# Kernel optimization log

Hardware: AMD Instinct MI355X
Metric: run time of the kernel (lower is better)

## Reference

```python
import jax, jax.numpy as jnp
import numpy as np

D = 1024      # d_model
ED = 2048     # d_inner
K = 4         # d_conv
N = 16        # d_state
R = 64        # dt_rank
E = 8         # num_experts
TOPK = 2      # num_experts_per_tok
FF = 2048     # mlp_size
EPS = 1e-6
B, L = 1, 2048


def setup_inputs() -> dict:
    key = jax.random.key(0)
    ks = jax.random.split(key, 12)
    def nrm(k, shape, scale=0.02):
        return jax.random.normal(k, shape, jnp.float32) * scale
    return {
        "x": jax.random.normal(ks[0], (B, L, D), jnp.float32),
        "rms1_w": jnp.ones((D,), jnp.float32),
        "rms2_w": jnp.ones((D,), jnp.float32),
        "W_in": nrm(ks[1], (2 * ED, D)),
        "conv_w": nrm(ks[2], (ED, 1, K), 0.1),
        "conv_b": jnp.zeros((ED,), jnp.float32),
        "W_xproj": nrm(ks[3], (R + 2 * N, ED)),
        "W_dt": nrm(ks[4], (ED, R), 0.1),
        "b_dt": jnp.full((ED,), -4.6, jnp.float32),  # softplus(-4.6) ~ 0.01 init dt
        "A_log": jnp.log(jnp.tile(jnp.arange(1, N + 1, dtype=jnp.float32), (ED, 1))),  # S4D-real init
        "D_skip": jnp.ones((ED,), jnp.float32),
        "W_out": nrm(ks[5], (D, ED)),
        "W_router": nrm(ks[6], (E, D)),
        "gate_w": nrm(ks[7], (E, FF, D)),
        "up_w": nrm(ks[8], (E, FF, D)),
        "down_w": nrm(ks[9], (E, D, FF)),
    }


def rmsnorm(x, w):
    return x * jax.lax.rsqrt(jnp.mean(x * x, -1, keepdims=True) + EPS) * w


def mamba(x, W_in, conv_w, conv_b, W_xproj, W_dt, b_dt, A_log, D_skip, W_out):
    Bb, Ll, _ = x.shape
    xm, z = jnp.split(x @ W_in.T, 2, axis=-1)                 # [B,L,ED] each
    # depthwise causal conv over time
    xc = jax.lax.conv_general_dilated(xm.transpose(0, 2, 1), conv_w, (1,), [(K - 1, 0)],
                                      feature_group_count=ED)  # [B,ED,L]
    xc = jax.nn.silu((xc + conv_b[None, :, None]).transpose(0, 2, 1))  # [B,L,ED]
    dt, Bm, Cm = jnp.split(xc @ W_xproj.T, [R, R + N], axis=-1)        # [B,L,R],[B,L,N],[B,L,N]
    delta = jax.nn.softplus(dt @ W_dt.T + b_dt)                        # [B,L,ED]
    A = -jnp.exp(A_log)                                                # [ED,N]
    dA = jnp.exp(delta[..., None] * A)                                 # [B,L,ED,N]
    dBx = delta[..., None] * Bm[:, :, None, :] * xc[..., None]         # [B,L,ED,N]

    def step(h, t):
        dA_t, dBx_t, C_t = t
        h = dA_t * h + dBx_t
        return h, jnp.einsum("ben,bn->be", h, C_t)

    h0 = jnp.zeros((Bb, ED, N), x.dtype)
    _, ys = jax.lax.scan(step, h0, (dA.transpose(1, 0, 2, 3), dBx.transpose(1, 0, 2, 3), Cm.transpose(1, 0, 2)))
    y = ys.transpose(1, 0, 2) + D_skip * xc
    y = y * jax.nn.silu(z)
    return y @ W_out.T


def moe(x2d, W_router, gate_w, up_w, down_w):
    logits = x2d @ W_router.T                                  # [T,E]
    probs = jax.nn.softmax(logits.astype(jnp.float32), -1)
    topw, sel = jax.lax.top_k(probs, TOPK)                     # NOTE: no renormalization (faithful)
    topw = topw.astype(x2d.dtype)
    wmat = jnp.sum(jax.nn.one_hot(sel, E, dtype=x2d.dtype) * topw[..., None], axis=1)  # [T,E]
    g = jnp.einsum("td,efd->tef", x2d, gate_w)
    u = jnp.einsum("td,efd->tef", x2d, up_w)
    h = jax.nn.silu(g) * u
    ye = jnp.einsum("tef,edf->ted", h, down_w)
    out = jnp.einsum("ted,te->td", ye, wmat)
    return out, logits


def reference(x, rms1_w, rms2_w, W_in, conv_w, conv_b, W_xproj, W_dt, b_dt, A_log,
              D_skip, W_out, W_router, gate_w, up_w, down_w):
    Bb, Ll, Dd = x.shape
    res = x
    h = rmsnorm(x, rms1_w)
    h = mamba(h, W_in, conv_w, conv_b, W_xproj, W_dt, b_dt, A_log, D_skip, W_out)
    x = res + h
    res = x
    h = rmsnorm(x, rms2_w)
    mo, logits = moe(h.reshape(-1, Dd), W_router, gate_w, up_w, down_w)
    x = res + mo.reshape(Bb, Ll, Dd)
    return (x, logits)
```

## Files before the change

### kernel.cpp

```cpp
#include <hip/hip_runtime.h>
#include <math.h>

typedef unsigned short u16;
typedef unsigned int   u32;
typedef __attribute__((ext_vector_type(8))) short bf16x8;
typedef __attribute__((ext_vector_type(4))) float f32x4;

constexpr int Tn=2048, Dm=1024, EDc=2048, Ns=16, Rr=64, NEx=8, FFc=2048;
constexpr int SCH=32, SNCH=Tn/SCH;
constexpr int MAXTM=40;
constexpr float LOG2E = 1.44269504f;

__device__ __forceinline__ float siluf(float x){ return __fdividef(x, 1.f + __expf(-x)); }
__device__ __forceinline__ u16 bfr(float f){
  u32 u = __float_as_uint(f);
  return (u16)((u + 0x7fffu + ((u>>16)&1u)) >> 16);
}
__device__ __forceinline__ float b2f(u16 h){ return __uint_as_float(((u32)h)<<16); }

__device__ __forceinline__ void gload16(const void* g, void* l){
  __builtin_amdgcn_global_load_lds((const __attribute__((address_space(1))) void*)g,
                                   (__attribute__((address_space(3))) void*)l, 16, 0, 0);
}

__global__ __launch_bounds__(256) void f2b_k(const float* __restrict__ in,
                                             u16* __restrict__ out, int n4){
  int i = blockIdx.x*256 + threadIdx.x;
  if (i >= n4) return;
  float4 v = ((const float4*)in)[i];
  u32 lo = (u32)bfr(v.x) | ((u32)bfr(v.y)<<16);
  u32 hi = (u32)bfr(v.z) | ((u32)bfr(v.w)<<16);
  ((uint2*)out)[i] = make_uint2(lo, hi);
}

__global__ __launch_bounds__(256) void f2b3_k(
    const float* __restrict__ g, const float* __restrict__ u,
    const float* __restrict__ d,
    u16* __restrict__ og, u16* __restrict__ ou, u16* __restrict__ od){
  const int BPW = (NEx*FFc*Dm/4)/256;
  int b = blockIdx.x;
  int which = b / BPW;
  int i = (b - which*BPW)*256 + threadIdx.x;
  const float* in = (which==0) ? g : (which==1) ? u : d;
  u16* out        = (which==0) ? og : (which==1) ? ou : od;
  float4 v = ((const float4*)in)[i];
  u32 lo = (u32)bfr(v.x) | ((u32)bfr(v.y)<<16);
  u32 hi = (u32)bfr(v.z) | ((u32)bfr(v.w)<<16);
  ((uint2*)out)[i] = make_uint2(lo, hi);
}

__global__ __launch_bounds__(256) void rmsnorm_k(const float* __restrict__ x,
                                                 const float* __restrict__ w,
                                                 u16* __restrict__ ob){
  int t = blockIdx.x;
  const float* xr = x + (size_t)t * Dm;
  float v[4]; float s = 0.f;
#pragma unroll
  for (int j = 0; j < 4; j++){ int d = threadIdx.x + j*256; v[j] = xr[d]; s += v[j]*v[j]; }
#pragma unroll
  for (int m = 1; m < 64; m <<= 1) s += __shfl_xor(s, m);
  __shared__ float red[4]; __shared__ float sb;
  int lane = threadIdx.x & 63, wv = threadIdx.x >> 6;
  if (lane == 0) red[wv] = s;
  __syncthreads();
  if (threadIdx.x == 0) sb = rsqrtf((red[0]+red[1]+red[2]+red[3]) * (1.f/Dm) + 1e-6f);
  __syncthreads();
  float sc = sb;
#pragma unroll
  for (int j = 0; j < 4; j++){
    int d = threadIdx.x + j*256;
    ob[(size_t)t*Dm + d] = bfr(v[j]*sc*w[d]);
  }
}

__global__ __launch_bounds__(256) void rms2red_k(
  const float* __restrict__ x, const float* __restrict__ P,
  const float* __restrict__ w,
  float* __restrict__ out, float* __restrict__ h2f, u16* __restrict__ h2b)
{
  int t = blockIdx.x, tid = threadIdx.x;
  const size_t S = (size_t)Tn*Dm;
  float v[4]; float s = 0.f;
#pragma unroll
  for (int j = 0; j < 4; j++){
    int d = tid + j*256;
    size_t idx = (size_t)t*Dm + d;
    float a = x[idx] + ((P[idx] + P[S+idx]) + (P[2*S+idx] + P[3*S+idx]));
    out[idx] = a; v[j] = a; s += a*a;
  }
#pragma unroll
  for (int m = 1; m < 64; m <<= 1) s += __shfl_xor(s, m);
  __shared__ float red[4]; __shared__ float sb;
  int lane = tid & 63, wv = tid >> 6;
  if (lane == 0) red[wv] = s;
  __syncthreads();
  if (tid == 0) sb = rsqrtf((red[0]+red[1]+red[2]+red[3]) * (1.f/Dm) + 1e-6f);
  __syncthreads();
  float sc = sb;
#pragma unroll
  for (int j = 0; j < 4; j++){
    int d = tid + j*256;
    float o = v[j]*sc*w[d];
    h2b[(size_t)t*Dm + d] = bfr(o);
    h2f[(size_t)t*Dm + d] = o;
  }
}

template<int EPI, int OB>
__global__ __launch_bounds__(512) void gemm_bb(
    const u16* __restrict__ A, int lda,
    const u16* __restrict__ B, int ldb,
    void* __restrict__ Cv, int ldc,
    int M, int N, int Ksl, const float* __restrict__ aux)
{
  __shared__ u16 As[2*4096], Bs[2*4096];
  int tid = threadIdx.x, lane = tid & 63, wid = tid >> 6;
  int wr = wid >> 2, wc = wid & 3;
  int n0 = blockIdx.x * 128, m0 = blockIdx.y * 128;
  int r = tid >> 2;
  int kk = ((tid & 3) ^ (r & 3)) * 8;
  size_t kbeg = (size_t)blockIdx.z * Ksl;
  const u16* Ag = A + (size_t)min(m0 + r, M-1)*lda + kbeg + kk;
  const u16* Bg = B + (size_t)min(n0 + r, N-1)*ldb + kbeg + kk;
  f32x4 acc[4][2] = {};
  int sw = ((lane>>4) ^ (lane&3)) * 8;
  int aoff[4], boff[2];
#pragma unroll
  for (int i = 0; i < 4; i++) aoff[i] = (wr*64 + i*16 + (lane&15))*32 + sw;
#pragma unroll
  for (int j = 0; j < 2; j++) boff[j] = (wc*32 + j*16 + (lane&15))*32 + sw;
  gload16(Ag, As + tid*8);
  gload16(Bg, Bs + tid*8);
  int NT = Ksl >> 5;
  for (int kt = 0; kt < NT; kt++){
    int cur = (kt & 1) * 4096;
    if (kt + 1 < NT){
      int nxt = 4096 - cur;
      gload16(Ag + (size_t)(kt+1)*32, As + nxt + tid*8);
      gload16(Bg + (size_t)(kt+1)*32, Bs + nxt + tid*8);
      asm volatile("s_waitcnt vmcnt(2)" ::: "memory");
    } else {
      asm volatile("s_waitcnt vmcnt(0)" ::: "memory");
    }
    __builtin_amdgcn_s_barrier();
    bf16x8 af[4], bv[2];
#pragma unroll
    for (int i = 0; i < 4; i++) af[i] = *(const bf16x8*)&As[cur + aoff[i]];
#pragma unroll
    for (int j = 0; j < 2; j++) bv[j] = *(const bf16x8*)&Bs[cur + boff[j]];
    asm volatile("s_waitcnt lgkmcnt(0)" ::: "memory");
    __builtin_amdgcn_sched_barrier(0);
    __builtin_amdgcn_s_barrier();
    __builtin_amdgcn_s_setprio(1);
#pragma unroll
    for (int i = 0; i < 4; i++)
#pragma unroll
      for (int j = 0; j < 2; j++)
        acc[i][j] = __builtin_amdgcn_mfma_f32_16x16x32_bf16(af[i], bv[j], acc[i][j], 0,0,0);
    __builtin_amdgcn_s_setprio(0);
  }
  float* Cf = (float*)Cv + (size_t)blockIdx.z * M * ldc;
  u16*   Cb = (u16*)Cv;
#pragma unroll
  for (int i = 0; i < 4; i++){
    int rbase = m0 + wr*64 + i*16 + ((lane>>4)<<2);
#pragma unroll
    for (int j = 0; j < 2; j++){
      int col = n0 + wc*32 + j*16 + (lane&15);
      if (col >= N) continue;
#pragma unroll
      for (int q = 0; q < 4; q++){
        int row = rbase + q;
        if (row >= M) continue;
        float v = acc[i][j][q];
        if (EPI == 1){ v += aux[col]; v = (v > 20.f) ? v : __logf(1.f + __expf(v)); }
        if (OB) Cb[(size_t)row*ldc + col] = bfr(v);
        else    Cf[(size_t)row*ldc + col] = v;
      }
    }
  }
}

__global__ __launch_bounds__(512) void gateup8(
    const u16* __restrict__ Aall,
    const u16* __restrict__ Wg, const u16* __restrict__ Wu,
    const int* __restrict__ cnt, const int* __restrict__ off,
    const int* __restrict__ bucket,
    const int* __restrict__ tmap, const int* __restrict__ ntot,
    u16* __restrict__ H)
{
  if ((int)blockIdx.y >= *ntot) return;
  int v = tmap[blockIdx.y];
  int e = v >> 16, m0 = (v & 0xFFFF) * 128;
  int Me = cnt[e];
  __shared__ u16 As[3*4096], Gs[3*4096], Us[3*4096];
  int tid = threadIdx.x, lane = tid & 63, wid = tid >> 6;
  int wr = wid >> 2, wc = wid & 3;
  int n0 = blockIdx.x * 128;
  int r = tid >> 2;
  int kk = ((tid & 3) ^ (r & 3)) * 8;
  int arow = bucket[e*Tn + min(m0 + r, Me-1)];
  const u16* Ag = Aall + (size_t)arow*Dm + kk;
  const u16* Gg = Wg + ((size_t)e*FFc + n0 + r)*Dm + kk;
  const u16* Ug = Wu + ((size_t)e*FFc + n0 + r)*Dm + kk;
  f32x4 ag[4][2] = {}, au[4][2] = {};
  int sw = ((lane>>4) ^ (lane&3)) * 8;
  int aoff[4], boff[2];
#pragma unroll
  for (int i = 0; i < 4; i++) aoff[i] = (wr*64 + i*16 + (lane&15))*32 + sw;
#pragma unroll
  for (int j = 0; j < 2; j++) boff[j] = (wc*32 + j*16 + (lane&15))*32 + sw;
  gload16(Ag,      As + tid*8);
  gload16(Gg,      Gs + tid*8);
  gload16(Ug,      Us + tid*8);
  gload16(Ag + 32, As + 4096 + tid*8);
  gload16(Gg + 32, Gs + 4096 + tid*8);
  gload16(Ug + 32, Us + 4096 + tid*8);
  const int NT = Dm >> 5;
  int cur = 0;
  for (int kt = 0; kt < NT; kt++){
    if (kt + 2 < NT){
      int nx2 = cur + 2*4096; if (nx2 >= 3*4096) nx2 -= 3*4096;
      gload16(Ag + (size_t)(kt+2)*32, As + nx2 + tid*8);
      gload16(Gg + (size_t)(kt+2)*32, Gs + nx2 + tid*8);
      gload16(Ug + (size_t)(kt+2)*32, Us + nx2 + tid*8);
      asm volatile("s_waitcnt vmcnt(6)" ::: "memory");
    } else if (kt + 1 < NT){
      asm volatile("s_waitcnt vmcnt(3)" ::: "memory");
    } else {
      asm volatile("s_waitcnt vmcnt(0)" ::: "memory");
    }
    __builtin_amdgcn_s_barrier();
    bf16x8 af[4], gf[2], uf[2];
#pragma unroll
    for (int i = 0; i < 4; i++) af[i] = *(const bf16x8*)&As[cur + aoff[i]];
#pragma unroll
    for (int j = 0; j < 2; j++){ gf[j] = *(const bf16x8*)&Gs[cur + boff[j]];
                                 uf[j] = *(const bf16x8*)&Us[cur + boff[j]]; }
    asm volatile("s_waitcnt lgkmcnt(0)" ::: "memory");
    __builtin_amdgcn_sched_barrier(0);
    __builtin_amdgcn_s_barrier();
    __builtin_amdgcn_s_setprio(1);
#pragma unroll
    for (int i = 0; i < 4; i++)
#pragma unroll
      for (int j = 0; j < 2; j++){
        ag[i][j] = __builtin_amdgcn_mfma_f32_16x16x32_bf16(af[i], gf[j], ag[i][j], 0,0,0);
        au[i][j] = __builtin_amdgcn_mfma_f32_16x16x32_bf16(af[i], uf[j], au[i][j], 0,0,0);
      }
    __builtin_amdgcn_s_setprio(0);
    cur += 4096; if (cur >= 3*4096) cur -= 3*4096;
  }
  int offe = off[e];
#pragma unroll
  for (int i = 0; i < 4; i++){
    int mb = m0 + wr*64 + i*16 + ((lane>>4)<<2);
#pragma unroll
    for (int j = 0; j < 2; j++){
      int col = n0 + wc*32 + j*16 + (lane&15);
#pragma unroll
      for (int q = 0; q < 4; q++){
        int m = mb + q;
        if (m >= Me) continue;
        float g = ag[i][j][q], u = au[i][j][q];
        H[(size_t)(offe + m)*FFc + col] = bfr(siluf(g)*u);
      }
    }
  }
}

__global__ __launch_bounds__(512) void down8(
    const u16* __restrict__ Hall, const u16* __restrict__ Wd,
    const int* __restrict__ cnt, const int* __restrict__ off,
    const int* __restrict__ tmap, const int* __restrict__ ntot,
    u16* __restrict__ Y)
{
  if ((int)blockIdx.y >= *ntot) return;
  int v = tmap[blockIdx.y];
  int e = v >> 16, m0 = (v & 0xFFFF) * 128;
  int Me = cnt[e];
  int offe = off[e];
  int kbeg = blockIdx.z * (FFc/2);
  const u16* A = Hall + (size_t)offe*FFc;
  const u16* B = Wd + (size_t)e*Dm*FFc;
  u16* C = Y + (size_t)blockIdx.z*(2*Tn)*Dm + (size_t)offe*Dm;
  __shared__ u16 As[3*4096], Bs[3*4096];
  int tid = threadIdx.x, lane = tid & 63, wid = tid >> 6;
  int wr = wid >> 2, wc = wid & 3;
  int n0 = blockIdx.x * 128;
  int r = tid >> 2;
  int kk = ((tid & 3) ^ (r & 3)) * 8;
  const u16* Ag = A + (size_t)min(m0 + r, Me-1)*FFc + kbeg + kk;
  const u16* Bg = B + (size_t)(n0 + r)*FFc + kbeg + kk;
  f32x4 acc[4][2] = {};
  int sw = ((lane>>4) ^ (lane&3)) * 8;
  int aoff[4], boff[2];
#pragma unroll
  for (int i = 0; i < 4; i++) aoff[i] = (wr*64 + i*16 + (lane&15))*32 + sw;
#pragma unroll
  for (int j = 0; j < 2; j++) boff[j] = (wc*32 + j*16 + (lane&15))*32 + sw;
  gload16(Ag,      As + tid*8);
  gload16(Bg,      Bs + tid*8);
  gload16(Ag + 32, As + 4096 + tid*8);
  gload16(Bg + 32, Bs + 4096 + tid*8);
  const int NT = (FFc/2) >> 5;
  int cur = 0;
  for (int kt = 0; kt < NT; kt++){
    if (kt + 2 < NT){
      int nx2 = cur + 2*4096; if (nx2 >= 3*4096) nx2 -= 3*4096;
      gload16(Ag + (size_t)(kt+2)*32, As + nx2 + tid*8);
      gload16(Bg + (size_t)(kt+2)*32, Bs + nx2 + tid*8);
      asm volatile("s_waitcnt vmcnt(4)" ::: "memory");
    } else if (kt + 1 < NT){
      asm volatile("s_waitcnt vmcnt(2)" ::: "memory");
    } else {
      asm volatile("s_waitcnt vmcnt(0)" ::: "memory");
    }
    __builtin_amdgcn_s_barrier();
    bf16x8 af[4], bv[2];
#pragma unroll
    for (int i = 0; i < 4; i++) af[i] = *(const bf16x8*)&As[cur + aoff[i]];
#pragma unroll
    for (int j = 0; j < 2; j++) bv[j] = *(const bf16x8*)&Bs[cur + boff[j]];
    asm volatile("s_waitcnt lgkmcnt(0)" ::: "memory");
    __builtin_amdgcn_sched_barrier(0);
    __builtin_amdgcn_s_barrier();
    __builtin_amdgcn_s_setprio(1);
#pragma unroll
    for (int i = 0; i < 4; i++)
#pragma unroll
      for (int j = 0; j < 2; j++)
        acc[i][j] = __builtin_amdgcn_mfma_f32_16x16x32_bf16(af[i], bv[j], acc[i][j], 0,0,0);
    __builtin_amdgcn_s_setprio(0);
    cur += 4096; if (cur >= 3*4096) cur -= 3*4096;
  }
#pragma unroll
  for (int i = 0; i < 4; i++){
    int mb = m0 + wr*64 + i*16 + ((lane>>4)<<2);
#pragma unroll
    for (int j = 0; j < 2; j++){
      int col = n0 + wc*32 + j*16 + (lane&15);
#pragma unroll
      for (int q = 0; q < 4; q++){
        int m = mb + q;
        if (m >= Me) continue;
        C[(size_t)m*Dm + col] = bfr(acc[i][j][q]);
      }
    }
  }
}

__global__ __launch_bounds__(256) void conv_k(const u16* __restrict__ xzb,
    const float* __restrict__ cw, const float* __restrict__ cb,
    u16* __restrict__ xc)
{
  int idx = blockIdx.x*256 + threadIdx.x;
  int t = idx >> 11, e = idx & (EDc - 1);
  float v = cb[e];
#pragma unroll
  for (int k = 0; k < 4; k++){
    int tt = t - 3 + k;
    if (tt >= 0) v += b2f(xzb[(size_t)tt*(2*EDc) + e]) * cw[e*4 + k];
  }
  xc[(size_t)t*EDc + e] = bfr(siluf(v));
}

__global__ __launch_bounds__(256) void xp_red(const float* __restrict__ part,
                                              float* __restrict__ xp,
                                              u16* __restrict__ dtA){
  int i = blockIdx.x*256 + threadIdx.x;
  const int S = Tn*96;
  float v = part[i] + part[S + i] + part[2*S + i] + part[3*S + i];
  xp[i] = v;
  int t = i / 96, c = i - t*96;
  if (c < Rr) dtA[t*Rr + c] = bfr(v);
}

__global__ __launch_bounds__(256) void scan_p1(
  const u16* __restrict__ delta, const u16* __restrict__ xc,
  const float* __restrict__ xp,  const float* __restrict__ A_log,
  float* __restrict__ hend, float* __restrict__ dsum)
{
  __shared__ u16 sdel[SCH*256], sxc[SCH*256];
  __shared__ float sB[SCH*16];
  int tid = threadIdx.x;
  int e0 = blockIdx.x*256, c = blockIdx.y, t0 = c*SCH;
#pragma unroll
  for (int i = 0; i < 4; i++){
    int f = (i*256+tid)*8;
    int t = f >> 8, e = f & 255;
    gload16(&delta[(size_t)(t0+t)*EDc + e0 + e], sdel + f);
    gload16(&xc  [(size_t)(t0+t)*EDc + e0 + e], sxc + f);
  }
  sB[tid]       = xp[(size_t)(t0 + (tid>>4))*96 + Rr + (tid&15)];
  sB[tid+256]   = xp[(size_t)(t0 + ((tid+256)>>4))*96 + Rr + (tid&15)];
  float a2[16];
  {
    const float* ar = &A_log[(size_t)(e0+tid)*16];
#pragma unroll
    for (int n = 0; n < 16; n++) a2[n] = -__expf(ar[n]) * LOG2E;
  }
  __syncthreads();
  float h[16] = {};
  float ds = 0.f;
  for (int t = 0; t < SCH; t++){
    float del = b2f(sdel[t*256 + tid]);
    float xv  = b2f(sxc [t*256 + tid]);
    ds += del;
    float dbx = del * xv;
    float4 b0 = *(const float4*)&sB[t*16];
    float4 b1 = *(const float4*)&sB[t*16+4];
    float4 b2 = *(const float4*)&sB[t*16+8];
    float4 b3 = *(const float4*)&sB[t*16+12];
    float bb[16] = {b0.x,b0.y,b0.z,b0.w, b1.x,b1.y,b1.z,b1.w,
                    b2.x,b2.y,b2.z,b2.w, b3.x,b3.y,b3.z,b3.w};
#pragma unroll
    for (int n = 0; n < 16; n++){
      float dA = exp2f(del * a2[n]);
      h[n] = fmaf(dA, h[n], dbx * bb[n]);
    }
  }
  float* hp = &hend[((size_t)c*EDc + e0 + tid)*16];
#pragma unroll
  for (int n = 0; n < 16; n += 4)
    *(float4*)&hp[n] = make_float4(h[n], h[n+1], h[n+2], h[n+3]);
  dsum[c*EDc + e0 + tid] = ds;
}

__global__ __launch_bounds__(256) void scan_p2(
  const float* __restrict__ hend, const float* __restrict__ dsum,
  const float* __restrict__ A_log, float* __restrict__ hin)
{
  int g = blockIdx.x*256 + threadIdx.x;
  int e = g >> 4;
  float a2 = -__expf(A_log[g]) * LOG2E;
  float h = 0.f;
  for (int c = 0; c < SNCH; c++){
    hin[(size_t)c*EDc*Ns + g] = h;
    float P = exp2f(a2 * dsum[c*EDc + e]);
    h = fmaf(P, h, hend[(size_t)c*EDc*Ns + g]);
  }
}

__global__ __launch_bounds__(256) void scan_p3(
  const u16* __restrict__ delta, const u16* __restrict__ xc,
  const float* __restrict__ xp,  const u16* __restrict__ xzb,
  const float* __restrict__ A_log, const float* __restrict__ D_skip,
  const float* __restrict__ hin,   u16* __restrict__ y2)
{
  __shared__ u16 sdel[SCH*256], sxc[SCH*256], sz[SCH*256];
  __shared__ float sB[SCH*16], sC[SCH*16];
  int tid = threadIdx.x;
  int e0 = blockIdx.x*256, c = blockIdx.y, t0 = c*SCH;
#pragma unroll
  for (int i = 0; i < 4; i++){
    int f = (i*256+tid)*8;
    int t = f >> 8, e = f & 255;
    gload16(&delta[(size_t)(t0+t)*EDc + e0 + e], sdel + f);
    gload16(&xc  [(size_t)(t0+t)*EDc + e0 + e], sxc + f);
    gload16(&xzb [(size_t)(t0+t)*(2*EDc) + EDc + e0 + e], sz + f);
  }
  {
    int f0 = tid, f1 = tid + 256;
    sB[f0] = xp[(size_t)(t0 + (f0>>4))*96 + Rr + (f0&15)];
    sB[f1] = xp[(size_t)(t0 + (f1>>4))*96 + Rr + (f1&15)];
    sC[f0] = xp[(size_t)(t0 + (f0>>4))*96 + Rr + Ns + (f0&15)];
    sC[f1] = xp[(size_t)(t0 + (f1>>4))*96 + Rr + Ns + (f1&15)];
  }
  float a2[16];
  {
    const float* ar = &A_log[(size_t)(e0+tid)*16];
#pragma unroll
    for (int n = 0; n < 16; n++) a2[n] = -__expf(ar[n]) * LOG2E;
  }
  float dsk = D_skip[e0 + tid];
  float h[16];
  {
    const float* hp = &hin[((size_t)c*EDc + e0 + tid)*16];
#pragma unroll
    for (int n = 0; n < 16; n += 4){
      float4 hv = *(const float4*)&hp[n];
      h[n] = hv.x; h[n+1] = hv.y; h[n+2] = hv.z; h[n+3] = hv.w;
    }
  }
  __syncthreads();
  for (int t = 0; t < SCH; t++){
    float del = b2f(sdel[t*256 + tid]);
    float xv  = b2f(sxc [t*256 + tid]);
    float zv  = b2f(sz  [t*256 + tid]);
    float dbx = del * xv;
    float4 b0 = *(const float4*)&sB[t*16];
    float4 b1 = *(const float4*)&sB[t*16+4];
    float4 b2 = *(const float4*)&sB[t*16+8];
    float4 b3 = *(const float4*)&sB[t*16+12];
    float bb[16] = {b0.x,b0.y,b0.z,b0.w, b1.x,b1.y,b1.z,b1.w,
                    b2.x,b2.y,b2.z,b2.w, b3.x,b3.y,b3.z,b3.w};
    float4 c0 = *(const float4*)&sC[t*16];
    float4 c1 = *(const float4*)&sC[t*16+4];
    float4 c2 = *(const float4*)&sC[t*16+8];
    float4 c3 = *(const float4*)&sC[t*16+12];
    float cc[16] = {c0.x,c0.y,c0.z,c0.w, c1.x,c1.y,c1.z,c1.w,
                    c2.x,c2.y,c2.z,c2.w, c3.x,c3.y,c3.z,c3.w};
    float p0 = 0.f, p1 = 0.f, p2 = 0.f, p3 = 0.f;
#pragma unroll
    for (int n = 0; n < 16; n += 4){
      float dA0 = exp2f(del * a2[n]);
      float dA1 = exp2f(del * a2[n+1]);
      float dA2 = exp2f(del * a2[n+2]);
      float dA3 = exp2f(del * a2[n+3]);
      h[n]   = fmaf(dA0, h[n],   dbx * bb[n]);
      h[n+1] = fmaf(dA1, h[n+1], dbx * bb[n+1]);
      h[n+2] = fmaf(dA2, h[n+2], dbx * bb[n+2]);
      h[n+3] = fmaf(dA3, h[n+3], dbx * bb[n+3]);
      p0 = fmaf(h[n],   cc[n],   p0);
      p1 = fmaf(h[n+1], cc[n+1], p1);
      p2 = fmaf(h[n+2], cc[n+2], p2);
      p3 = fmaf(h[n+3], cc[n+3], p3);
    }
    float p = (p0 + p1) + (p2 + p3);
    y2[(size_t)(t0+t)*EDc + e0 + tid] = bfr((p + dsk*xv) * siluf(zv));
  }
}

__global__ __launch_bounds__(256) void route_k(
  const float* __restrict__ h2, const float* __restrict__ Wr,
  float* __restrict__ logits_out,
  int* __restrict__ cnt, int* __restrict__ bucket,
  int* __restrict__ tok_e, int* __restrict__ tok_idx, float* __restrict__ tok_w)
{
  int t = blockIdx.x, tid = threadIdx.x;
  float p[8] = {};
#pragma unroll
  for (int j = 0; j < 4; j++){
    int d = tid + j*256;
    float xv = h2[(size_t)t*Dm + d];
#pragma unroll
    for (int e = 0; e < 8; e++) p[e] += xv * Wr[e*Dm + d];
  }
#pragma unroll
  for (int e = 0; e < 8; e++)
#pragma unroll
    for (int m = 1; m < 64; m <<= 1) p[e] += __shfl_xor(p[e], m);
  __shared__ float part[4][8];
  __shared__ float lg[8];
  int lane = tid & 63, wv = tid >> 6;
  if (lane == 0)
#pragma unroll
    for (int e = 0; e < 8; e++) part[wv][e] = p[e];
  __syncthreads();
  if (tid < 8){
    float v = part[0][tid]+part[1][tid]+part[2][tid]+part[3][tid];
    lg[tid] = v;
    logits_out[(size_t)t*8 + tid] = v;
  }
  __syncthreads();
  if (tid == 0){
    float mx = lg[0];
#pragma unroll
    for (int e = 1; e < 8; e++) mx = fmaxf(mx, lg[e]);
    float ex[8], s = 0.f;
#pragma unroll
    for (int e = 0; e < 8; e++){ ex[e] = expf(lg[e] - mx); s += ex[e]; }
    float inv = 1.f / s;
    int i0 = 0; float b0 = ex[0]*inv;
#pragma unroll
    for (int e = 1; e < 8; e++){ float pe = ex[e]*inv; if (pe > b0){ b0 = pe; i0 = e; } }
    int i1 = -1; float b1 = -1e30f;
#pragma unroll
    for (int e = 0; e < 8; e++){ if (e == i0) continue; float pe = ex[e]*inv; if (pe > b1){ b1 = pe; i1 = e; } }
    int k0 = atomicAdd(&cnt[i0], 1); bucket[i0*Tn + k0] = t;
    int k1 = atomicAdd(&cnt[i1], 1); bucket[i1*Tn + k1] = t;
    tok_e[2*t] = i0;   tok_idx[2*t] = k0;   tok_w[2*t] = b0;
    tok_e[2*t+1] = i1; tok_idx[2*t+1] = k1; tok_w[2*t+1] = b1;
  }
}

__global__ void prefix_k(const int* __restrict__ cnt, int* __restrict__ off,
                         int* __restrict__ tmap, int* __restrict__ ntot){
  if (threadIdx.x == 0 && blockIdx.x == 0){
    int s = 0;
    for (int e = 0; e < NEx; e++){ off[e] = s; s += cnt[e]; }
    int nt = 0;
    for (int e = 0; e < NEx; e++){
      int tiles = (cnt[e] + 127) >> 7;
      for (int tm = 0; tm < tiles; tm++) tmap[nt++] = (e << 16) | tm;
    }
    *ntot = nt;
  }
}

__global__ __launch_bounds__(256) void combine_k(float* __restrict__ out,
    const u16* __restrict__ Y, const int* __restrict__ off,
    const int* __restrict__ tok_e, const int* __restrict__ tok_idx,
    const float* __restrict__ tok_w)
{
  int t = blockIdx.x, tid = threadIdx.x;
  const size_t S2 = (size_t)(2*Tn)*Dm;
  int e0 = tok_e[2*t],   e1 = tok_e[2*t+1];
  size_t r0 = (size_t)(off[e0] + tok_idx[2*t])*Dm;
  size_t r1 = (size_t)(off[e1] + tok_idx[2*t+1])*Dm;
  float w0 = tok_w[2*t], w1 = tok_w[2*t+1];
#pragma unroll
  for (int j = 0; j < 4; j++){
    int d = tid + j*256;
    float y0 = b2f(Y[r0 + d]) + b2f(Y[S2 + r0 + d]);
    float y1 = b2f(Y[r1 + d]) + b2f(Y[S2 + r1 + d]);
    out[(size_t)t*Dm + d] += w0*y0 + w1*y1;
  }
}

extern "C" void kernel_launch(void* const* d_in, const int* in_sizes, int n_in,
                              void* d_out, int out_size, void* d_ws, size_t ws_size,
                              hipStream_t stream) {
  const float* x      = (const float*)d_in[0];
  const float* rms1_w = (const float*)d_in[1];
  const float* rms2_w = (const float*)d_in[2];
  const float* W_in   = (const float*)d_in[3];
  const float* conv_w = (const float*)d_in[4];
  const float* conv_b = (const float*)d_in[5];
  const float* W_xprj = (const float*)d_in[6];
  const float* W_dt   = (const float*)d_in[7];
  const float* b_dt   = (const float*)d_in[8];
  const float* A_log  = (const float*)d_in[9];
  const float* D_skip = (const float*)d_in[10];
  const float* W_out  = (const float*)d_in[11];
  const float* W_rt   = (const float*)d_in[12];
  const float* gate_w = (const float*)d_in[13];
  const float* up_w   = (const float*)d_in[14];
  const float* down_w = (const float*)d_in[15];

  float* out        = (float*)d_out;
  float* logits_out = out + (size_t)Tn*Dm;

  uint8_t* base = (uint8_t*)d_ws;
  size_t o = 0;
  auto alloc = [&](size_t bytes) -> void* {
    void* p = base + o;
    o = (o + bytes + 255) & ~(size_t)255;
    return p;
  };
  float* h2f   = (float*)alloc((size_t)Tn*Dm*4);
  u16*   h2b   = (u16*)  alloc((size_t)Tn*Dm*2);
  u16*   hmoe  = (u16*)  alloc((size_t)2*Tn*FFc*2);
  u16*   yslot = (u16*)  alloc((size_t)2*(2*Tn)*Dm*2);
  int*   cnt     = (int*)alloc(64);
  int*   off     = (int*)alloc(64);
  int*   ntot    = (int*)alloc(64);
  int*   tmap    = (int*)alloc(MAXTM*4 + 192);
  int*   bucket  = (int*)alloc((size_t)NEx*Tn*4);
  int*   tok_e   = (int*)alloc((size_t)2*Tn*4);
  int*   tok_idx = (int*)alloc((size_t)2*Tn*4);
  float* tok_w   = (float*)alloc((size_t)2*Tn*4);
  size_t oz = o;
  u16*   xzb   = (u16*)  alloc((size_t)Tn*2*EDc*2);
  u16*   delta = (u16*)  alloc((size_t)Tn*EDc*2);
  u16*   xc    = (u16*)  alloc((size_t)Tn*EDc*2);
  u16*   y2    = (u16*)  alloc((size_t)Tn*EDc*2);
  u16*   h1b   = (u16*)  alloc((size_t)Tn*Dm*2);
  u16*   dtA   = (u16*)  alloc((size_t)Tn*Rr*2);
  float* xp    = (float*)alloc((size_t)Tn*96*4);
  float* xp_part=(float*)alloc((size_t)4*Tn*96*4);
  float* hend  = (float*)alloc((size_t)SNCH*EDc*Ns*4);
  float* hin   = (float*)alloc((size_t)SNCH*EDc*Ns*4);
  float* dsum  = (float*)alloc((size_t)SNCH*EDc*4);
  float* wpart = (float*)xzb;
  u16* wgate = (u16*)(base + oz);
  u16* wup   = wgate + (size_t)NEx*FFc*Dm;
  u16* wdown = wup   + (size_t)NEx*FFc*Dm;
  u16* wbin  = (u16*)yslot;
  u16* wbout = wbin + (size_t)2*EDc*Dm;
  u16* wxp   = (u16*)hmoe;
  u16* wdt   = wxp + (size_t)96*EDc;

  f2b_k<<<(2*EDc*Dm/4)/256, 256, 0, stream>>>(W_in,   wbin,  2*EDc*Dm/4);
  f2b_k<<<(Dm*EDc/4)/256,   256, 0, stream>>>(W_out,  wbout, Dm*EDc/4);
  f2b_k<<<(96*EDc/4)/256,   256, 0, stream>>>(W_xprj, wxp,   96*EDc/4);
  f2b_k<<<(EDc*Rr/4)/256,   256, 0, stream>>>(W_dt,   wdt,   EDc*Rr/4);
  rmsnorm_k<<<Tn, 256, 0, stream>>>(x, rms1_w, h1b);
  gemm_bb<0,1><<<dim3(32,16,1), 512, 0, stream>>>(h1b, Dm, wbin, Dm, xzb, 2*EDc, Tn, 2*EDc, Dm, nullptr);
  conv_k<<<(Tn*EDc)/256, 256, 0, stream>>>(xzb, conv_w, conv_b, xc);
  gemm_bb<0,0><<<dim3(1,16,4), 512, 0, stream>>>(xc, EDc, wxp, EDc, xp_part, 96, Tn, 96, EDc/4, nullptr);
  xp_red<<<(Tn*96)/256, 256, 0, stream>>>(xp_part, xp, dtA);
  gemm_bb<1,1><<<dim3(16,16,1), 512, 0, stream>>>(dtA, Rr, wdt, Rr, delta, EDc, Tn, EDc, Rr, b_dt);
  scan_p1<<<dim3(EDc/256, SNCH), 256, 0, stream>>>(delta, xc, xp, A_log, hend, dsum);
  scan_p2<<<EDc*Ns/256, 256, 0, stream>>>(hend, dsum, A_log, hin);
  scan_p3<<<dim3(EDc/256, SNCH), 256, 0, stream>>>(delta, xc, xp, xzb, A_log, D_skip, hin, y2);
  gemm_bb<0,0><<<dim3(8,16,4), 512, 0, stream>>>(y2, EDc, wbout, EDc, wpart, Dm, Tn, Dm, EDc/4, nullptr);
  rms2red_k<<<Tn, 256, 0, stream>>>(x, wpart, rms2_w, out, h2f, h2b);
  f2b3_k<<<3*((NEx*FFc*Dm/4)/256), 256, 0, stream>>>(gate_w, up_w, down_w, wgate, wup, wdown);
  hipMemsetAsync(cnt, 0, 32, stream);
  route_k<<<Tn, 256, 0, stream>>>(h2f, W_rt, logits_out, cnt, bucket, tok_e, tok_idx, tok_w);
  prefix_k<<<1, 64, 0, stream>>>(cnt, off, tmap, ntot);
  gateup8<<<dim3(16, MAXTM), 512, 0, stream>>>(h2b, wgate, wup, cnt, off, bucket, tmap, ntot, hmoe);
  down8<<<dim3(8, MAXTM, 2), 512, 0, stream>>>(hmoe, wdown, cnt, off, tmap, ntot, yslot);
  combine_k<<<Tn, 256, 0, stream>>>(out, yslot, off, tok_e, tok_idx, tok_w);
}
```

Baseline: 391.5 us.

## Enlarge MoE grouped GEMM M-tile to 256 rows with 64-wide warp N tiles

The gate/up and down expert GEMMs now use 256-row token tiles instead of 128. The warp layout becomes 4x2 with each warp computing a 64x64 sub-tile, and the A staging buffer doubles. The prefix kernel builds tiles of 256 and the grid shrinks to match. The goal is to halve how often expert weights are re-streamed per token tile and to raise MFMA work per LDS load. The cost is more padding waste per expert, fewer blocks to fill the GPU, and higher register and LDS pressure.

```diff
diff --git a/kernel.cpp b/kernel.cpp
--- a/kernel.cpp
+++ b/kernel.cpp
@@ -9,6 +9,7 @@
 constexpr int Tn=2048, Dm=1024, EDc=2048, Ns=16, Rr=64, NEx=8, FFc=2048;
 constexpr int SCH=32, SNCH=Tn/SCH;
 constexpr int MAXTM=40;
+constexpr int MAXTM2=24;
 constexpr float LOG2E = 1.44269504f;
 
 __device__ __forceinline__ float siluf(float x){ return __fdividef(x, 1.f + __expf(-x)); }
@@ -181,7 +182,7 @@
   }
 }
 
-__global__ __launch_bounds__(512) void gateup8(
+__global__ __launch_bounds__(512, 2) void gateup8(
     const u16* __restrict__ Aall,
     const u16* __restrict__ Wg, const u16* __restrict__ Wu,
     const int* __restrict__ cnt, const int* __restrict__ off,
@@ -191,52 +192,57 @@
 {
   if ((int)blockIdx.y >= *ntot) return;
   int v = tmap[blockIdx.y];
-  int e = v >> 16, m0 = (v & 0xFFFF) * 128;
+  int e = v >> 16, m0 = (v & 0xFFFF) * 256;
   int Me = cnt[e];
-  __shared__ u16 As[3*4096], Gs[3*4096], Us[3*4096];
+  __shared__ u16 As[3*8192], Gs[3*4096], Us[3*4096];
   int tid = threadIdx.x, lane = tid & 63, wid = tid >> 6;
-  int wr = wid >> 2, wc = wid & 3;
+  int wr = wid >> 1, wc = wid & 1;
   int n0 = blockIdx.x * 128;
   int r = tid >> 2;
   int kk = ((tid & 3) ^ (r & 3)) * 8;
-  int arow = bucket[e*Tn + min(m0 + r, Me-1)];
-  const u16* Ag = Aall + (size_t)arow*Dm + kk;
+  int arow  = bucket[e*Tn + min(m0 + r,       Me-1)];
+  int arow2 = bucket[e*Tn + min(m0 + 128 + r, Me-1)];
+  const u16* Ag  = Aall + (size_t)arow *Dm + kk;
+  const u16* Ag2 = Aall + (size_t)arow2*Dm + kk;
   const u16* Gg = Wg + ((size_t)e*FFc + n0 + r)*Dm + kk;
   const u16* Ug = Wu + ((size_t)e*FFc + n0 + r)*Dm + kk;
-  f32x4 ag[4][2] = {}, au[4][2] = {};
+  f32x4 ag[4][4] = {}, au[4][4] = {};
   int sw = ((lane>>4) ^ (lane&3)) * 8;
-  int aoff[4], boff[2];
+  int aoff[4], boff[4];
 #pragma unroll
   for (int i = 0; i < 4; i++) aoff[i] = (wr*64 + i*16 + (lane&15))*32 + sw;
 #pragma unroll
-  for (int j = 0; j < 2; j++) boff[j] = (wc*32 + j*16 + (lane&15))*32 + sw;
-  gload16(Ag,      As + tid*8);
-  gload16(Gg,      Gs + tid*8);
-  gload16(Ug,      Us + tid*8);
-  gload16(Ag + 32, As + 4096 + tid*8);
-  gload16(Gg + 32, Gs + 4096 + tid*8);
-  gload16(Ug + 32, Us + 4096 + tid*8);
+  for (int j = 0; j < 4; j++) boff[j] = (wc*64 + j*16 + (lane&15))*32 + sw;
   const int NT = Dm >> 5;
+  gload16(Ag,       As + tid*8);
+  gload16(Ag2,      As + 4096 + tid*8);
+  gload16(Gg,       Gs + tid*8);
+  gload16(Ug,       Us + tid*8);
+  gload16(Ag  + 32, As + 8192 + tid*8);
+  gload16(Ag2 + 32, As + 8192 + 4096 + tid*8);
+  gload16(Gg  + 32, Gs + 4096 + tid*8);
+  gload16(Ug  + 32, Us + 4096 + tid*8);
   int cur = 0;
   for (int kt = 0; kt < NT; kt++){
     if (kt + 2 < NT){
-      int nx2 = cur + 2*4096; if (nx2 >= 3*4096) nx2 -= 3*4096;
-      gload16(Ag + (size_t)(kt+2)*32, As + nx2 + tid*8);
-      gload16(Gg + (size_t)(kt+2)*32, Gs + nx2 + tid*8);
-      gload16(Ug + (size_t)(kt+2)*32, Us + nx2 + tid*8);
-      asm volatile("s_waitcnt vmcnt(6)" ::: "memory");
+      int nx = cur + 16384; if (nx >= 24576) nx -= 24576;
+      gload16(Ag  + (size_t)(kt+2)*32, As + nx + tid*8);
+      gload16(Ag2 + (size_t)(kt+2)*32, As + nx + 4096 + tid*8);
+      gload16(Gg  + (size_t)(kt+2)*32, Gs + (nx>>1) + tid*8);
+      gload16(Ug  + (size_t)(kt+2)*32, Us + (nx>>1) + tid*8);
+      asm volatile("s_waitcnt vmcnt(8)" ::: "memory");
     } else if (kt + 1 < NT){
-      asm volatile("s_waitcnt vmcnt(3)" ::: "memory");
+      asm volatile("s_waitcnt vmcnt(4)" ::: "memory");
     } else {
       asm volatile("s_waitcnt vmcnt(0)" ::: "memory");
     }
     __builtin_amdgcn_s_barrier();
-    bf16x8 af[4], gf[2], uf[2];
+    bf16x8 af[4], gf[4], uf[4];
 #pragma unroll
     for (int i = 0; i < 4; i++) af[i] = *(const bf16x8*)&As[cur + aoff[i]];
 #pragma unroll
-    for (int j = 0; j < 2; j++){ gf[j] = *(const bf16x8*)&Gs[cur + boff[j]];
-                                 uf[j] = *(const bf16x8*)&Us[cur + boff[j]]; }
+    for (int j = 0; j < 4; j++){ gf[j] = *(const bf16x8*)&Gs[(cur>>1) + boff[j]];
+                                 uf[j] = *(const bf16x8*)&Us[(cur>>1) + boff[j]]; }
     asm volatile("s_waitcnt lgkmcnt(0)" ::: "memory");
     __builtin_amdgcn_sched_barrier(0);
     __builtin_amdgcn_s_barrier();
@@ -244,20 +250,20 @@
 #pragma unroll
     for (int i = 0; i < 4; i++)
 #pragma unroll
-      for (int j = 0; j < 2; j++){
+      for (int j = 0; j < 4; j++){
         ag[i][j] = __builtin_amdgcn_mfma_f32_16x16x32_bf16(af[i], gf[j], ag[i][j], 0,0,0);
         au[i][j] = __builtin_amdgcn_mfma_f32_16x16x32_bf16(af[i], uf[j], au[i][j], 0,0,0);
       }
     __builtin_amdgcn_s_setprio(0);
-    cur += 4096; if (cur >= 3*4096) cur -= 3*4096;
+    cur += 8192; if (cur >= 24576) cur -= 24576;
   }
   int offe = off[e];
 #pragma unroll
   for (int i = 0; i < 4; i++){
     int mb = m0 + wr*64 + i*16 + ((lane>>4)<<2);
 #pragma unroll
-    for (int j = 0; j < 2; j++){
-      int col = n0 + wc*32 + j*16 + (lane&15);
+    for (int j = 0; j < 4; j++){
+      int col = n0 + wc*64 + j*16 + (lane&15);
 #pragma unroll
       for (int q = 0; q < 4; q++){
         int m = mb + q;
@@ -269,7 +275,7 @@
   }
 }
 
-__global__ __launch_bounds__(512) void down8(
+__global__ __launch_bounds__(512, 2) void down8(
     const u16* __restrict__ Hall, const u16* __restrict__ Wd,
     const int* __restrict__ cnt, const int* __restrict__ off,
     const int* __restrict__ tmap, const int* __restrict__ ntot,
@@ -277,51 +283,54 @@
 {
   if ((int)blockIdx.y >= *ntot) return;
   int v = tmap[blockIdx.y];
-  int e = v >> 16, m0 = (v & 0xFFFF) * 128;
+  int e = v >> 16, m0 = (v & 0xFFFF) * 256;
   int Me = cnt[e];
   int offe = off[e];
   int kbeg = blockIdx.z * (FFc/2);
   const u16* A = Hall + (size_t)offe*FFc;
-  const u16* B = Wd + (size_t)e*Dm*FFc;
   u16* C = Y + (size_t)blockIdx.z*(2*Tn)*Dm + (size_t)offe*Dm;
-  __shared__ u16 As[3*4096], Bs[3*4096];
+  __shared__ u16 As[3*8192], Bs[3*4096];
   int tid = threadIdx.x, lane = tid & 63, wid = tid >> 6;
-  int wr = wid >> 2, wc = wid & 3;
+  int wr = wid >> 1, wc = wid & 1;
   int n0 = blockIdx.x * 128;
   int r = tid >> 2;
   int kk = ((tid & 3) ^ (r & 3)) * 8;
-  const u16* Ag = A + (size_t)min(m0 + r, Me-1)*FFc + kbeg + kk;
-  const u16* Bg = B + (size_t)(n0 + r)*FFc + kbeg + kk;
-  f32x4 acc[4][2] = {};
+  const u16* Ag  = A + (size_t)min(m0 + r,       Me-1)*FFc + kbeg + kk;
+  const u16* Ag2 = A + (size_t)min(m0 + 128 + r, Me-1)*FFc + kbeg + kk;
+  const u16* Bg = Wd + (size_t)e*Dm*FFc + (size_t)(n0 + r)*FFc + kbeg + kk;
+  f32x4 acc[4][4] = {};
   int sw = ((lane>>4) ^ (lane&3)) * 8;
-  int aoff[4], boff[2];
+  int aoff[4], boff[4];
 #pragma unroll
   for (int i = 0; i < 4; i++) aoff[i] = (wr*64 + i*16 + (lane&15))*32 + sw;
 #pragma unroll
-  for (int j = 0; j < 2; j++) boff[j] = (wc*32 + j*16 + (lane&15))*32 + sw;
-  gload16(Ag,      As + tid*8);
-  gload16(Bg,      Bs + tid*8);
-  gload16(Ag + 32, As + 4096 + tid*8);
-  gload16(Bg + 32, Bs + 4096 + tid*8);
+  for (int j = 0; j < 4; j++) boff[j] = (wc*64 + j*16 + (lane&15))*32 + sw;
   const int NT = (FFc/2) >> 5;
+  gload16(Ag,       As + tid*8);
+  gload16(Ag2,      As + 4096 + tid*8);
+  gload16(Bg,       Bs + tid*8);
+  gload16(Ag  + 32, As + 8192 + tid*8);
+  gload16(Ag2 + 32, As + 8192 + 4096 + tid*8);
+  gload16(Bg  + 32, Bs + 4096 + tid*8);
   int cur = 0;
   for (int kt = 0; kt < NT; kt++){
     if (kt + 2 < NT){
-      int nx2 = cur + 2*4096; if (nx2 >= 3*4096) nx2 -= 3*4096;
-      gload16(Ag + (size_t)(kt+2)*32, As + nx2 + tid*8);
-      gload16(Bg + (size_t)(kt+2)*32, Bs + nx2 + tid*8);
-      asm volatile("s_waitcnt vmcnt(4)" ::: "memory");
+      int nx = cur + 16384; if (nx >= 24576) nx -= 24576;
+      gload16(Ag  + (size_t)(kt+2)*32, As + nx + tid*8);
+      gload16(Ag2 + (size_t)(kt+2)*32, As + nx + 4096 + tid*8);
+      gload16(Bg  + (size_t)(kt+2)*32, Bs + (nx>>1) + tid*8);
+      asm volatile("s_waitcnt vmcnt(6)" ::: "memory");
     } else if (kt + 1 < NT){
-      asm volatile("s_waitcnt vmcnt(2)" ::: "memory");
+      asm volatile("s_waitcnt vmcnt(3)" ::: "memory");
     } else {
       asm volatile("s_waitcnt vmcnt(0)" ::: "memory");
     }
     __builtin_amdgcn_s_barrier();
-    bf16x8 af[4], bv[2];
+    bf16x8 af[4], bv[4];
 #pragma unroll
     for (int i = 0; i < 4; i++) af[i] = *(const bf16x8*)&As[cur + aoff[i]];
 #pragma unroll
-    for (int j = 0; j < 2; j++) bv[j] = *(const bf16x8*)&Bs[cur + boff[j]];
+    for (int j = 0; j < 4; j++) bv[j] = *(const bf16x8*)&Bs[(cur>>1) + boff[j]];
     asm volatile("s_waitcnt lgkmcnt(0)" ::: "memory");
     __builtin_amdgcn_sched_barrier(0);
     __builtin_amdgcn_s_barrier();
@@ -329,17 +338,17 @@
 #pragma unroll
     for (int i = 0; i < 4; i++)
 #pragma unroll
-      for (int j = 0; j < 2; j++)
+      for (int j = 0; j < 4; j++)
         acc[i][j] = __builtin_amdgcn_mfma_f32_16x16x32_bf16(af[i], bv[j], acc[i][j], 0,0,0);
     __builtin_amdgcn_s_setprio(0);
-    cur += 4096; if (cur >= 3*4096) cur -= 3*4096;
+    cur += 8192; if (cur >= 24576) cur -= 24576;
   }
 #pragma unroll
   for (int i = 0; i < 4; i++){
     int mb = m0 + wr*64 + i*16 + ((lane>>4)<<2);
 #pragma unroll
-    for (int j = 0; j < 2; j++){
-      int col = n0 + wc*32 + j*16 + (lane&15);
+    for (int j = 0; j < 4; j++){
+      int col = n0 + wc*64 + j*16 + (lane&15);
 #pragma unroll
       for (int q = 0; q < 4; q++){
         int m = mb + q;
@@ -582,7 +591,7 @@
     for (int e = 0; e < NEx; e++){ off[e] = s; s += cnt[e]; }
     int nt = 0;
     for (int e = 0; e < NEx; e++){
-      int tiles = (cnt[e] + 127) >> 7;
+      int tiles = (cnt[e] + 255) >> 8;
       for (int tm = 0; tm < tiles; tm++) tmap[nt++] = (e << 16) | tm;
     }
     *ntot = nt;
@@ -691,7 +700,7 @@
   hipMemsetAsync(cnt, 0, 32, stream);
   route_k<<<Tn, 256, 0, stream>>>(h2f, W_rt, logits_out, cnt, bucket, tok_e, tok_idx, tok_w);
   prefix_k<<<1, 64, 0, stream>>>(cnt, off, tmap, ntot);
-  gateup8<<<dim3(16, MAXTM), 512, 0, stream>>>(h2b, wgate, wup, cnt, off, bucket, tmap, ntot, hmoe);
-  down8<<<dim3(8, MAXTM, 2), 512, 0, stream>>>(hmoe, wdown, cnt, off, tmap, ntot, yslot);
+  gateup8<<<dim3(16, MAXTM2), 512, 0, stream>>>(h2b, wgate, wup, cnt, off, bucket, tmap, ntot, hmoe);
+  down8<<<dim3(8, MAXTM2, 2), 512, 0, stream>>>(hmoe, wdown, cnt, off, tmap, ntot, yslot);
   combine_k<<<Tn, 256, 0, stream>>>(out, yslot, off, tok_e, tok_idx, tok_w);
 }
```

New measurement: 411.7 us. +5.2%, slower.
